# Kernel tuning notes

Measured on AMD Instinct MI355X. Metric: run time of the kernel, lower is better.

## Reference

```python
import jax, jax.numpy as jnp
import numpy as np
from jax import lax

C = 128; HEADS = 16; HD = 8; EPS = 1e-5

def _conv3x3(x, w):
    return lax.conv_general_dilated(x, w, (1, 1), 'SAME', dimension_numbers=('NCHW', 'OIHW', 'NCHW'))

def _cbr3(x, w, g, b):
    # Conv3x3 + BatchNorm(eval, running stats folded -> per-channel affine) + ReLU
    return jax.nn.relu(_conv3x3(x, w) * g[:, None, None] + b[:, None, None])

def _cbr1(x, w, g, b):
    y = jnp.einsum('bchw,oc->bohw', x, w)
    return jax.nn.relu(y * g[:, None, None] + b[:, None, None])

def _ln(t, g, b):
    mu = t.mean(-1, keepdims=True)
    va = ((t - mu) ** 2).mean(-1, keepdims=True)
    return (t - mu) / jnp.sqrt(va + EPS) * g + b

def _gconv1x1(xf, w, b, groups):
    # grouped 1x1 conv on flattened spatial dim: xf [B,Cin,N], w [Cout, Cin//groups]
    B, Cin, N = xf.shape
    Cout = w.shape[0]
    y = jnp.einsum('bgcn,goc->bgon', xf.reshape(B, groups, Cin // groups, N),
                   w.reshape(groups, Cout // groups, Cin // groups))
    return y.reshape(B, Cout, N) + b[:, None]

def _ss_softmax(a):
    # sign * sqrt(|a| + 1e-5) then softmax (GISSA's custom transform)
    a = jnp.sign(a) * jnp.sqrt(jnp.abs(a) + 1e-5)
    return jax.nn.softmax(a, axis=-1)

def _gissa(ximg, qkv_w, qkv_b, g, b, qkv2_w, qkv2_b):
    B, Cc, H, W = ximg.shape
    N = H * W
    xf = ximg.reshape(B, Cc, N)
    qkv = _gconv1x1(xf, qkv_w, qkv_b, HEADS).reshape(B, 3, HEADS, HD, N)
    q, k, v = qkv[:, 0], qkv[:, 1], qkv[:, 2]
    attn = _ss_softmax(jnp.einsum('bhdn,bhen->bhde', q, k) * HD ** -0.5)  # [B,h,hd,hd]
    x1 = jnp.einsum('bhde,bhen->bhdn', attn, v).reshape(B, Cc, N) + xf
    x1 = x1.reshape(B, HEADS, HD, N).transpose(0, 2, 1, 3).reshape(B, Cc, N)  # channel shuffle
    y = x1 * g[:, None] + b[:, None]  # BatchNorm eval affine
    xr = jax.nn.relu(y)
    qkv2 = _gconv1x1(xr, qkv2_w, qkv2_b, HD).reshape(B, 3, HD, HEADS, N)
    q2, k2, v2 = qkv2[:, 0], qkv2[:, 1], qkv2[:, 2]
    attn2 = _ss_softmax(jnp.einsum('bdhn,bdgn->bdhg', q2, k2) * HEADS ** -0.5)  # [B,hd,h,h]
    o = jnp.einsum('bdhg,bdgn->bdhn', attn2, v2).transpose(0, 2, 1, 3).reshape(B, Cc, N) + y
    return o.reshape(B, Cc, H, W)

def _swsa_calc(ximg, pi_w, pi_b, g, b, po_w, po_b):
    B, Cc, H, W = ximg.shape
    t = jnp.einsum('bcn,oc->bon', ximg.reshape(B, Cc, H * W), pi_w) + pi_b[:, None]
    t = t * g[:, None] + b[:, None]  # BN affine
    q = t[:, :Cc].transpose(0, 2, 1)  # [B,N,C]
    v = t[:, Cc:].transpose(0, 2, 1)
    atn = jax.nn.softmax(jnp.einsum('bnc,bmc->bnm', q, q) * Cc ** -0.5, axis=-1)
    y = jnp.einsum('bnm,bmc->bnc', atn, v).transpose(0, 2, 1)  # [B,C,N]
    y = (jnp.einsum('bcn,oc->bon', y, po_w) + po_b[:, None]).reshape(B, Cc, H, W)
    return y, atn

def _swsa_reuse(ximg, atn, pi_w, pi_b, g, b, po_w, po_b):
    B, Cc, H, W = ximg.shape
    t = jnp.einsum('bcn,oc->bon', ximg.reshape(B, Cc, H * W), pi_w) + pi_b[:, None]
    t = t * g[:, None] + b[:, None]
    v = t.transpose(0, 2, 1)
    y = (jnp.einsum('bnm,bmc->bnc', atn, v) * Cc ** -0.5).transpose(0, 2, 1)
    return (jnp.einsum('bcn,oc->bon', y, po_w) + po_b[:, None]).reshape(B, Cc, H, W)

def _forward(x, ssfe_w, ssfe_g, ssfe_b, cc_w, cc_g, cc_b, ln1_g, ln1_b, qkv_w, qkv_b, gbn_g, gbn_b, qkv2_w, qkv2_b, ln2_g, ln2_b, mlp_w1, mlp_b1, mlp_w2, mlp_b2, cs_w, cs_g, cs_b, lfe0_w, lfe0_g, lfe0_b, s0_pi_w, s0_pi_b, s0_bn_g, s0_bn_b, s0_po_w, s0_po_b, lfe1_w, lfe1_g, lfe1_b, s1_pi_w, s1_pi_b, s1_bn_g, s1_bn_b, s1_po_w, s1_po_b, lamuda, fc_w):
    B, Cin, H, W = x.shape
    N = H * W
    # SSFE stem (approximated as Conv3x3+BN+ReLU; source def unavailable)
    xs = _cbr3(x, ssfe_w, ssfe_g, ssfe_b)
    # channel branch: 1x1 CBR + SIT (LN -> GISSA -> residual -> LN -> MLP -> residual)
    xc = _cbr1(xs, cc_w, cc_g, cc_b)
    t = xc.reshape(B, C, N).transpose(0, 2, 1)  # [B,N,C]
    cur = _ln(t, ln1_g, ln1_b).transpose(0, 2, 1).reshape(B, C, H, W)
    t = t + _gissa(cur, qkv_w, qkv_b, gbn_g, gbn_b, qkv2_w, qkv2_b).reshape(B, C, N).transpose(0, 2, 1)
    h = _ln(t, ln2_g, ln2_b)
    h = jax.nn.gelu(h @ mlp_w1.T + mlp_b1, approximate=False) @ mlp_w2.T + mlp_b2
    t = t + h
    xc = t.transpose(0, 2, 1).reshape(B, C, H, W)
    # spatial branch: 3x3 CBR + SCA (LFE + SWSA with attention reuse)
    xp = _cbr3(xs, cs_w, cs_g, cs_b)
    xp = _cbr3(xp, lfe0_w, lfe0_g, lfe0_b) + xp
    y, atn = _swsa_calc(xp, s0_pi_w, s0_pi_b, s0_bn_g, s0_bn_b, s0_po_w, s0_po_b)
    xp = y + xp
    xp = _cbr3(xp, lfe1_w, lfe1_g, lfe1_b) + xp
    xp = _swsa_reuse(xp, atn, s1_pi_w, s1_pi_b, s1_bn_g, s1_bn_b, s1_po_w, s1_po_b) + xp
    lmd = jax.nn.sigmoid(lamuda[0])
    out = lmd * xc + (1.0 - lmd) * xp
    return out.mean(axis=(2, 3)) @ fc_w.T  # global avg pool + fc (dropout p=0 for HUST2013)

def setup_inputs():
    ks = iter(jax.random.split(jax.random.key(0), 64))
    def rn(shape, scale=0.05):
        return jax.random.normal(next(ks), shape, jnp.float32) * scale
    ones = lambda *s: jnp.ones(s, jnp.float32)
    zeros = lambda *s: jnp.zeros(s, jnp.float32)
    return dict(
        x=jax.random.normal(next(ks), (32, 144, 32, 32), jnp.float32),
        ssfe_w=rn((144, 144, 3, 3)), ssfe_g=ones(144), ssfe_b=zeros(144),
        cc_w=rn((128, 144)), cc_g=ones(128), cc_b=zeros(128),
        ln1_g=ones(128), ln1_b=zeros(128),
        qkv_w=rn((384, 8)), qkv_b=zeros(384),
        gbn_g=ones(128), gbn_b=zeros(128),
        qkv2_w=rn((384, 16)), qkv2_b=zeros(384),
        ln2_g=ones(128), ln2_b=zeros(128),
        mlp_w1=rn((512, 128)), mlp_b1=zeros(512),
        mlp_w2=rn((128, 512)), mlp_b2=zeros(128),
        cs_w=rn((128, 144, 3, 3)), cs_g=ones(128), cs_b=zeros(128),
        lfe0_w=rn((128, 128, 3, 3)), lfe0_g=ones(128), lfe0_b=zeros(128),
        s0_pi_w=rn((256, 128)), s0_pi_b=zeros(256), s0_bn_g=ones(256), s0_bn_b=zeros(256),
        s0_po_w=rn((128, 128)), s0_po_b=zeros(128),
        lfe1_w=rn((128, 128, 3, 3)), lfe1_g=ones(128), lfe1_b=zeros(128),
        s1_pi_w=rn((128, 128)), s1_pi_b=zeros(128), s1_bn_g=ones(128), s1_bn_b=zeros(128),
        s1_po_w=rn((128, 128)), s1_po_b=zeros(128),
        lamuda=jnp.full((1,), 0.5, jnp.float32),
        fc_w=rn((16, 128)),
    )

def reference(x, ssfe_w, ssfe_g, ssfe_b, cc_w, cc_g, cc_b, ln1_g, ln1_b, qkv_w, qkv_b, gbn_g, gbn_b, qkv2_w, qkv2_b, ln2_g, ln2_b, mlp_w1, mlp_b1, mlp_w2, mlp_b2, cs_w, cs_g, cs_b, lfe0_w, lfe0_g, lfe0_b, s0_pi_w, s0_pi_b, s0_bn_g, s0_bn_b, s0_po_w, s0_po_b, lfe1_w, lfe1_g, lfe1_b, s1_pi_w, s1_pi_b, s1_bn_g, s1_bn_b, s1_po_w, s1_po_b, lamuda, fc_w):
    return _forward(x, ssfe_w, ssfe_g, ssfe_b, cc_w, cc_g, cc_b, ln1_g, ln1_b, qkv_w, qkv_b, gbn_g, gbn_b, qkv2_w, qkv2_b, ln2_g, ln2_b, mlp_w1, mlp_b1, mlp_w2, mlp_b2, cs_w, cs_g, cs_b, lfe0_w, lfe0_g, lfe0_b, s0_pi_w, s0_pi_b, s0_bn_g, s0_bn_b, s0_po_w, s0_po_b, lfe1_w, lfe1_g, lfe1_b, s1_pi_w, s1_pi_b, s1_bn_g, s1_bn_b, s1_po_w, s1_po_b, lamuda, fc_w)
```

## Files before the change

### kernel.cpp

```cpp
#include <hip/hip_runtime.h>
#include <math.h>


static constexpr int NPIX = 1024;

typedef __attribute__((ext_vector_type(8))) short bf16x8;
typedef __attribute__((ext_vector_type(4))) float f32x4;
typedef __attribute__((ext_vector_type(8))) unsigned short u16x8;
typedef __attribute__((ext_vector_type(4))) unsigned short u16x4;

static __device__ __forceinline__ unsigned short f2bf(float f) {
    unsigned u = __builtin_bit_cast(unsigned, f);
    unsigned r = (u + 0x7fffu + ((u >> 16) & 1u)) >> 16;
    return (unsigned short)r;
}
static __device__ __forceinline__ float bf2f(unsigned short u) {
    unsigned v = ((unsigned)u) << 16;
    return __builtin_bit_cast(float, v);
}

__global__ __launch_bounds__(256) void prepack_convs(
    const float* __restrict__ ssfe_w, const float* __restrict__ cs_w,
    const float* __restrict__ lfe0_w, const float* __restrict__ lfe1_w,
    unsigned short* __restrict__ wssfe, unsigned short* __restrict__ wcs,
// ... 188 lines not shown
    __shared__ unsigned short X[130 * PITCH];
    const int tid = threadIdx.x;
    const int b = blockIdx.x, gr = blockIdx.y;
    const int pbase = gr << 6;
    const int gbase = pbase - 33;
    const int wid = tid >> 6, lane = tid & 63;
    const int ll = lane & 15, lq = lane >> 4;
    const int co0w = wid << 5;
    const unsigned short* xb = xT + ((size_t)b << 10) * CINP;

#pragma unroll 1
    for (int idx = tid; idx < 130 * NCHK; idx += 256) {
        const int row = idx / NCHK;
        const int chunk = idx - row * NCHK;
        const int gp = gbase + row;
        u16x8 v = {};
        if (gp >= 0 && gp < 1024)
            v = *(const u16x8*)(xb + (size_t)gp * CINP + chunk * 8);
        *(u16x8*)&X[row * PITCH + chunk * 8] = v;
    }
    __syncthreads();

    f32x4 acc[2][4];
#pragma unroll
    for (int i = 0; i < 2; ++i)
#pragma unroll
        for (int j = 0; j < 4; ++j)
#pragma unroll
            for (int r = 0; r < 4; ++r) acc[i][j][r] = 0.f;

#pragma unroll
    for (int tap = 0; tap < 9; ++tap) {
        const int soff = (tap / 3) * 32 + (tap % 3);
        const int dx = tap % 3;
#pragma unroll
        for (int kc = 0; kc < CINP / 32; ++kc) {
            bf16x8 bfv[4];
#pragma unroll
            for (int j = 0; j < 4; ++j) {
                const int p = j * 16 + ll;
                bf16x8 v = *(const bf16x8*)&X[(p + soff) * PITCH + kc * 32 + lq * 8];
                const bool zed = (dx == 0 && (j & 1) == 0 && ll == 0) ||
                                 (dx == 2 && (j & 1) == 1 && ll == 15);
                if (zed) { bf16x8 z = {}; v = z; }
                bfv[j] = v;
            }
            const unsigned short* wb =
                wrep + ((size_t)tap * Cout + co0w) * CINP + kc * 32 + lq * 8;
#pragma unroll
            for (int i = 0; i < 2; ++i) {
                bf16x8 af = *(const bf16x8*)(wb + (size_t)(i * 16 + ll) * CINP);
#pragma unroll
                for (int j = 0; j < 4; ++j)
                    acc[i][j] = __builtin_amdgcn_mfma_f32_16x16x32_bf16(
                        af, bfv[j], acc[i][j], 0, 0, 0);
            }
        }
    }

#pragma unroll
    for (int i = 0; i < 2; ++i) {
        const int cob = co0w + i * 16 + lq * 4;
        float gv[4], bv[4];
#pragma unroll
        for (int r = 0; r < 4; ++r) { gv[r] = g[cob + r]; bv[r] = bb[cob + r]; }
#pragma unroll
        for (int j = 0; j < 4; ++j) {
            const int px = pbase + j * 16 + ll;
            const size_t rowT = ((size_t)((b << 10) + px)) << 7;
            u16x4 rv = {};
            if (resT) rv = *(const u16x4*)(resT + rowT + cob);
            u16x4 tp;
#pragma unroll
            for (int r = 0; r < 4; ++r) {
                float v = fmaxf(acc[i][j][r] * gv[r] + bv[r], 0.f);
                if (resT) v += bf2f(rv[r]);
                tp[r] = f2bf(v);
            }
            *(u16x4*)(outT + rowT + cob) = tp;
        }
    }
}

template <int KP>
__global__ __launch_bounds__(256) void lin_mfma_kernel(
    const unsigned short* __restrict__ xT, const unsigned short* __restrict__ wbf,
    const float* __restrict__ bias0, const float* __restrict__ g,
    const float* __restrict__ bb, const unsigned short* __restrict__ resT,
    float* __restrict__ outF, unsigned short* __restrict__ outBF,
    unsigned short* __restrict__ outT, int do_relu)
{
    const int tid = threadIdx.x;
    const int b = blockIdx.x;
    const int n0 = blockIdx.y << 6;
    const int wid = tid >> 6, lane = tid & 63;
    const int ll = lane & 15, lq = lane >> 4;
    const unsigned short* xb = xT + (size_t)((b << 10) + n0) * KP;

    f32x4 acc[2][4];
#pragma unroll
    for (int i = 0; i < 2; ++i)
#pragma unroll
        for (int j = 0; j < 4; ++j)
#pragma unroll
            for (int r = 0; r < 4; ++r) acc[i][j][r] = 0.f;

#pragma unroll
    for (int kk = 0; kk < KP / 32; ++kk) {
        bf16x8 af[2], bfv[4];
#pragma unroll
        for (int i = 0; i < 2; ++i)
            af[i] = *(const bf16x8*)(wbf + (size_t)(wid * 32 + i * 16 + ll) * KP + kk * 32 + lq * 8);
#pragma unroll
        for (int j = 0; j < 4; ++j)
            bfv[j] = *(const bf16x8*)(xb + (size_t)(j * 16 + ll) * KP + kk * 32 + lq * 8);
#pragma unroll
        for (int i = 0; i < 2; ++i)
#pragma unroll
            for (int j = 0; j < 4; ++j)
                acc[i][j] = __builtin_amdgcn_mfma_f32_16x16x32_bf16(af[i], bfv[j], acc[i][j], 0, 0, 0);
    }

#pragma unroll
    for (int i = 0; i < 2; ++i) {
        const int cob = wid * 32 + i * 16 + lq * 4;
        float b0v[4], gv[4], bv[4];
#pragma unroll
        for (int r = 0; r < 4; ++r) {
            b0v[r] = bias0 ? bias0[cob + r] : 0.f;
            gv[r] = g ? g[cob + r] : 1.f;
            bv[r] = g ? bb[cob + r] : 0.f;
        }
#pragma unroll
        for (int j = 0; j < 4; ++j) {
            const int px = n0 + j * 16 + ll;
            const size_t rowT = ((size_t)((b << 10) + px)) << 7;
            u16x4 rv = {};
            if (resT) rv = *(const u16x4*)(resT + rowT + cob);
            u16x4 tp;
#pragma unroll
            for (int r = 0; r < 4; ++r) {
                const int co = cob + r;
                float v = acc[i][j][r] + b0v[r];
                v = v * gv[r] + bv[r];
                if (do_relu) v = fmaxf(v, 0.f);
                if (resT) v += bf2f(rv[r]);
                if (outF) outF[((size_t)((b << 7) + co) << 10) + px] = v;
                unsigned short h = f2bf(v);
                if (outBF) outBF[((size_t)((b << 7) + co) << 10) + px] = h;
                tp[r] = h;
            }
            if (outT) *(u16x4*)(outT + rowT + cob) = tp;
        }
    }
}

__global__ __launch_bounds__(256) void pi0_kernel(
    const unsigned short* __restrict__ xT, const unsigned short* __restrict__ wbf,
    const float* __restrict__ bias0, const float* __restrict__ g,
    const float* __restrict__ bb, unsigned short* __restrict__ qTout,
    unsigned short* __restrict__ vout)
{
    const int tid = threadIdx.x;
    const int b = blockIdx.x;
    const int n0 = blockIdx.y << 6;
    const int wid = tid >> 6, lane = tid & 63;
    const int ll = lane & 15, lq = lane >> 4;
    const int co0 = wid << 6;
    const unsigned short* xb = xT + (size_t)((b << 10) + n0) * 128;

    f32x4 acc[4][4];
#pragma unroll
    for (int i = 0; i < 4; ++i)
#pragma unroll
        for (int j = 0; j < 4; ++j)
#pragma unroll
            for (int r = 0; r < 4; ++r) acc[i][j][r] = 0.f;

#pragma unroll
    for (int kk = 0; kk < 4; ++kk) {
        bf16x8 af[4], bfv[4];
#pragma unroll
        for (int i = 0; i < 4; ++i)
            af[i] = *(const bf16x8*)(wbf + (size_t)(co0 + i * 16 + ll) * 128 + kk * 32 + lq * 8);
#pragma unroll
        for (int j = 0; j < 4; ++j)
            bfv[j] = *(const bf16x8*)(xb + (size_t)(j * 16 + ll) * 128 + kk * 32 + lq * 8);
#pragma unroll
        for (int i = 0; i < 4; ++i)
#pragma unroll
            for (int j = 0; j < 4; ++j)
                acc[i][j] = __builtin_amdgcn_mfma_f32_16x16x32_bf16(af[i], bfv[j], acc[i][j], 0, 0, 0);
    }

#pragma unroll
    for (int i = 0; i < 4; ++i) {
        const int cob = co0 + i * 16 + lq * 4;
        float b0v[4], gv[4], bv[4];
#pragma unroll
        for (int r = 0; r < 4; ++r) {
            b0v[r] = bias0[cob + r];
            gv[r] = g[cob + r];
            bv[r] = bb[cob + r];
        }
#pragma unroll
        for (int j = 0; j < 4; ++j) {
            const int px = n0 + j * 16 + ll;
            float vv[4];
#pragma unroll
            for (int r = 0; r < 4; ++r)
                vv[r] = (acc[i][j][r] + b0v[r]) * gv[r] + bv[r];
            if (wid < 2) {
                u16x4 tp;
#pragma unroll
                for (int r = 0; r < 4; ++r) tp[r] = f2bf(vv[r]);
                *(u16x4*)(qTout + (((size_t)((b << 10) + px)) << 7) + cob) = tp;
            } else {
#pragma unroll
                for (int r = 0; r < 4; ++r)
                    vout[((size_t)(b * 128 + cob - 128 + r) << 10) + px] = f2bf(vv[r]);
            }
        }
    }
}

__global__ __launch_bounds__(256) void ln_kernel(
    const float* __restrict__ in, const float* __restrict__ g,
    const float* __restrict__ bb, unsigned short* __restrict__ out_bf,
    unsigned short* __restrict__ outT)
{
    const int tid = threadIdx.x;
    const int b = blockIdx.x >> 2;
    const int n = ((blockIdx.x & 3) << 8) + tid;
    const float* ib = in + ((size_t)b << 17) + n;
    float s = 0.f, sq = 0.f;
#pragma unroll 8
    for (int c = 0; c < 128; ++c) {
        float v = ib[(size_t)c << 10];
        s += v;
        sq += v * v;
    }
    const float mu = s * 0.0078125f;
    const float r = rsqrtf(sq * 0.0078125f - mu * mu + 1e-5f);
    unsigned short* obf = out_bf + ((size_t)b << 17) + n;
    unsigned short* oT = outT + (((size_t)b << 10) + n) * 128;
#pragma unroll 2
    for (int c0 = 0; c0 < 128; c0 += 8) {
        u16x8 pk;
#pragma unroll
        for (int e = 0; e < 8; ++e) {
            const int c = c0 + e;
            float v = ib[(size_t)c << 10];
            float y = (v - mu) * r * g[c] + bb[c];
            unsigned short h = f2bf(y);
            obf[(size_t)c << 10] = h;
            pk[e] = h;
        }
        *(u16x8*)(oT + c0) = pk;
    }
}

__global__ __launch_bounds__(256) void gram_kernel(
    const unsigned short* __restrict__ Xbf, float* __restrict__ G)
{
    __shared__ unsigned short Xs[128 * 128];
    const int tid = threadIdx.x;
    const int b = blockIdx.x >> 2;
    const int rg = blockIdx.x & 3;
    const int wid = tid >> 6, lane = tid & 63;
    const int lq = lane >> 4, ll = lane & 15;
    const unsigned short* Xb = Xbf + ((size_t)b << 17);

    f32x4 acc[2][2];
#pragma unroll
    for (int mi = 0; mi < 2; ++mi)
#pragma unroll
        for (int ci = 0; ci < 2; ++ci)
#pragma unroll
            for (int r = 0; r < 4; ++r) acc[mi][ci][r] = 0.f;

#pragma unroll 1
    for (int nt = 0; nt < 8; ++nt) {
        const int n0 = nt << 7;
#pragma unroll
        for (int p = 0; p < 8; ++p) {
            const int ch = (p << 4) + (tid >> 4);
            const int seg = (tid & 15) << 3;
            *(u16x8*)&Xs[ch * 128 + (seg ^ ((ch & 7) << 3))] =
                *(const u16x8*)(Xb + ((size_t)ch << 10) + n0 + seg);
        }
        __syncthreads();
#pragma unroll
        for (int ks = 0; ks < 4; ++ks) {
            bf16x8 af[2], bf_[2];
#pragma unroll
            for (int mi = 0; mi < 2; ++mi) {
                const int ar = (rg << 5) + mi * 16 + ll;
                af[mi] = *(const bf16x8*)&Xs[ar * 128 + ((ks * 32 + lq * 8) ^ ((ar & 7) << 3))];
            }
#pragma unroll
            for (int ci = 0; ci < 2; ++ci) {
                const int br = (wid << 5) + ci * 16 + ll;
                bf_[ci] = *(const bf16x8*)&Xs[br * 128 + ((ks * 32 + lq * 8) ^ ((br & 7) << 3))];
            }
// ... 358 lines not shown
                for (int r = 0; r < 4; ++r) acc[i][j][r] = 0.f;
#pragma unroll
        for (int kk = 0; kk < 4; ++kk) {
            bf16x8 af[4], bfr[4];
#pragma unroll
            for (int i = 0; i < 4; ++i)
                af[i] = *(const bf16x8*)(w1bf + (size_t)(hidbase + i * 16 + lr) * 128 + kk * 32 + lk * 8);
#pragma unroll
            for (int j = 0; j < 4; ++j) {
                const int px = j * 16 + lr;
                bfr[j] = *(const bf16x8*)(xnb + px * 256 + ((kk * 64 + lk * 16) ^ ((px & 7) << 4)));
            }
#pragma unroll
            for (int i = 0; i < 4; ++i)
#pragma unroll
                for (int j = 0; j < 4; ++j)
                    acc[i][j] = __builtin_amdgcn_mfma_f32_16x16x32_bf16(af[i], bfr[j], acc[i][j], 0, 0, 0);
        }
#pragma unroll
        for (int i = 0; i < 4; ++i) {
            const int hid0 = hidbase + i * 16 + lk * 4;
            float bi[4];
#pragma unroll
            for (int r = 0; r < 4; ++r) bi[r] = b1[hid0 + r];
#pragma unroll
            for (int j = 0; j < 4; ++j) {
                const int px = j * 16 + lr;
                u16x4 pk;
#pragma unroll
                for (int r = 0; r < 4; ++r) {
                    float x = acc[i][j][r] + bi[r];
                    float u = 1.5957691f * x * (1.f + 0.044715f * x * x);
                    float gv = x / (1.f + __expf(-u));
                    pk[r] = f2bf(gv);
                }
                *(u16x4*)(hb + px * 1024 + ((hid0 * 2) ^ ((px & 7) << 4))) = pk;
            }
        }
    }
    __syncthreads();

    f32x4 acc2[2][4];
#pragma unroll
    for (int i = 0; i < 2; ++i)
#pragma unroll
        for (int j = 0; j < 4; ++j)
#pragma unroll
            for (int r = 0; r < 4; ++r) acc2[i][j][r] = 0.f;
#pragma unroll 2
    for (int ks = 0; ks < 16; ++ks) {
        bf16x8 af[2], bfr[4];
#pragma unroll
        for (int i = 0; i < 2; ++i)
            af[i] = *(const bf16x8*)(w2bf + (size_t)((wid << 5) + i * 16 + lr) * 512 + ks * 32 + lk * 8);
#pragma unroll
        for (int j = 0; j < 4; ++j) {
            const int px = j * 16 + lr;
            bfr[j] = *(const bf16x8*)(hb + px * 1024 + ((ks * 64 + lk * 16) ^ ((px & 7) << 4)));
        }
#pragma unroll
        for (int i = 0; i < 2; ++i)
#pragma unroll
            for (int j = 0; j < 4; ++j)
                acc2[i][j] = __builtin_amdgcn_mfma_f32_16x16x32_bf16(af[i], bfr[j], acc2[i][j], 0, 0, 0);
    }
#pragma unroll
    for (int i = 0; i < 2; ++i) {
        const int cb = (wid << 5) + i * 16 + lk * 4;
        float b2v[4];
#pragma unroll
        for (int r = 0; r < 4; ++r) b2v[r] = b2[cb + r];
#pragma unroll
        for (int j = 0; j < 4; ++j) {
            const int px = j * 16 + lr;
#pragma unroll
            for (int r = 0; r < 4; ++r) {
                const size_t off = ((size_t)(cb + r) << 10) + px;
                tb[off] += acc2[i][j][r] + b2v[r];
            }
        }
    }
}

__global__ __launch_bounds__(256) void swsa_po_kernel(
    const unsigned short* __restrict__ qT, const unsigned short* __restrict__ vbf,
    const unsigned short* __restrict__ wpo, const float* __restrict__ po_b,
    const unsigned short* __restrict__ resT,
    unsigned short* __restrict__ outT, float* __restrict__ outF, float fscale)
{
    __shared__ unsigned short K_lds[128 * 128];
    __shared__ unsigned short V_lds[128 * 128];
    const int tid = threadIdx.x;
    const int b = blockIdx.x & 31;
    const int n0 = (blockIdx.x >> 5) << 6;
    const int wid = tid >> 6, lane = tid & 63;
    const int lq = lane >> 4, ll = lane & 15;
    const unsigned short* qTb = qT + ((size_t)b << 17);
    const unsigned short* vb = vbf + ((size_t)b << 17);

    bf16x8 aq[4];
    {
        const int row = n0 + wid * 16 + ll;
#pragma unroll
        for (int kk = 0; kk < 4; ++kk)
            aq[kk] = *(const bf16x8*)(qTb + ((size_t)row << 7) + kk * 32 + lq * 8);
    }

    float mrun[4], lrun[4];
#pragma unroll
    for (int i = 0; i < 4; ++i) { mrun[i] = -INFINITY; lrun[i] = 0.f; }
    f32x4 yacc[8];
#pragma unroll
    for (int cj = 0; cj < 8; ++cj)
#pragma unroll
        for (int r = 0; r < 4; ++r) yacc[cj][r] = 0.f;

#pragma unroll 1
    for (int mt = 0; mt < 8; ++mt) {
        const int m0 = mt << 7;
        for (int ch = tid; ch < 2048; ch += 256) {
            const int rr = ch >> 4, e0 = (ch & 15) << 3;
            const int sw = (rr & 7) << 3;
            *(u16x8*)&K_lds[rr * 128 + (e0 ^ sw)] =
                *(const u16x8*)(qTb + ((size_t)(m0 + rr) << 7) + e0);
            *(u16x8*)&V_lds[rr * 128 + (e0 ^ sw)] =
                *(const u16x8*)(vb + ((size_t)rr << 10) + m0 + e0);
        }
        __syncthreads();

        f32x4 sacc[8];
#pragma unroll
        for (int j = 0; j < 8; ++j)
#pragma unroll
            for (int r = 0; r < 4; ++r) sacc[j][r] = 0.f;
#pragma unroll
        for (int j = 0; j < 8; ++j) {
            const int ml = j * 16 + ll;
            const int swk = (ml & 7) << 3;
#pragma unroll
            for (int kk = 0; kk < 4; ++kk) {
                bf16x8 bk = *(const bf16x8*)&K_lds[ml * 128 + ((kk * 32 + lq * 8) ^ swk)];
                sacc[j] = __builtin_amdgcn_mfma_f32_16x16x32_bf16(aq[kk], bk, sacc[j], 0, 0, 0);
            }
        }
        __syncthreads();

        float pmax[4];
#pragma unroll
        for (int i = 0; i < 4; ++i) pmax[i] = -INFINITY;
#pragma unroll
        for (int j = 0; j < 8; ++j)
#pragma unroll
            for (int r = 0; r < 4; ++r) {
                float s = sacc[j][r] * 0.08838834764831845f;
                sacc[j][r] = s;
                pmax[r] = fmaxf(pmax[r], s);
            }
        float alpha[4];
#pragma unroll
        for (int i = 0; i < 4; ++i) {
            float m = pmax[i];
            m = fmaxf(m, __shfl_xor(m, 1));
            m = fmaxf(m, __shfl_xor(m, 2));
            m = fmaxf(m, __shfl_xor(m, 4));
            m = fmaxf(m, __shfl_xor(m, 8));
            const float mn = fmaxf(mrun[i], m);
            alpha[i] = __expf(mrun[i] - mn);
            mrun[i] = mn;
        }
        float psum[4];
#pragma unroll
        for (int r = 0; r < 4; ++r) {
            const int nbw = wid * 16 + lq * 4 + r;
            const int sw4 = ((nbw >> 2) & 3) << 4;
            const float mn = mrun[r];
            float ps = 0.f;
#pragma unroll
            for (int j = 0; j < 8; ++j) {
                float p = __expf(sacc[j][r] - mn);
                ps += p;
                K_lds[nbw * 128 + ((j * 16 + ll) ^ sw4)] = f2bf(p);
            }
            psum[r] = ps;
        }
#pragma unroll
        for (int i = 0; i < 4; ++i) {
            float s = psum[i];
            s += __shfl_xor(s, 1);
            s += __shfl_xor(s, 2);
            s += __shfl_xor(s, 4);
            s += __shfl_xor(s, 8);
            lrun[i] = lrun[i] * alpha[i] + s;
        }
#pragma unroll
        for (int cj = 0; cj < 8; ++cj)
#pragma unroll
            for (int r = 0; r < 4; ++r) yacc[cj][r] *= alpha[r];

        bf16x8 ap[4];
        {
            const int nb = wid * 16 + ll;
            const int sw4 = ((nb >> 2) & 3) << 4;
#pragma unroll
            for (int mk = 0; mk < 4; ++mk)
                ap[mk] = *(const bf16x8*)&K_lds[nb * 128 + ((mk * 32 + lq * 8) ^ sw4)];
        }
#pragma unroll
        for (int cj = 0; cj < 8; ++cj) {
            const int cl = cj * 16 + ll;
            const int sw = (cl & 7) << 3;
#pragma unroll
            for (int mk = 0; mk < 4; ++mk) {
                bf16x8 bv = *(const bf16x8*)&V_lds[cl * 128 + ((mk * 32 + lq * 8) ^ sw)];
                yacc[cj] = __builtin_amdgcn_mfma_f32_16x16x32_bf16(ap[mk], bv, yacc[cj], 0, 0, 0);
            }
        }
        __syncthreads();
    }

    {
        float inv[4];
#pragma unroll
        for (int r = 0; r < 4; ++r) inv[r] = fscale / lrun[r];
        const int rw0 = wid * 16 + lq * 4;
#pragma unroll
        for (int cj = 0; cj < 8; ++cj) {
            const int c = cj * 16 + ll;
#pragma unroll
            for (int r = 0; r < 4; ++r) {
                const int row = rw0 + r;
                const int sw4 = ((row >> 2) & 3) << 4;
                K_lds[row * 128 + (c ^ sw4)] = f2bf(yacc[cj][r] * inv[r]);
            }
        }
    }
    __syncthreads();

    f32x4 acc2[2][4];
#pragma unroll
    for (int i = 0; i < 2; ++i)
#pragma unroll
        for (int j = 0; j < 4; ++j)
#pragma unroll
            for (int r = 0; r < 4; ++r) acc2[i][j][r] = 0.f;
#pragma unroll
    for (int kk = 0; kk < 4; ++kk) {
        bf16x8 af[2], bfv[4];
#pragma unroll
        for (int i = 0; i < 2; ++i)
            af[i] = *(const bf16x8*)(wpo + (size_t)(wid * 32 + i * 16 + ll) * 128 + kk * 32 + lq * 8);
#pragma unroll
        for (int j = 0; j < 4; ++j) {
            const int row = j * 16 + ll;
            const int sw4 = ((row >> 2) & 3) << 4;
            bfv[j] = *(const bf16x8*)&K_lds[row * 128 + ((kk * 32 + lq * 8) ^ sw4)];
        }
#pragma unroll
        for (int i = 0; i < 2; ++i)
#pragma unroll
            for (int j = 0; j < 4; ++j)
                acc2[i][j] = __builtin_amdgcn_mfma_f32_16x16x32_bf16(af[i], bfv[j], acc2[i][j], 0, 0, 0);
    }

#pragma unroll
    for (int i = 0; i < 2; ++i) {
        const int cob = wid * 32 + i * 16 + lq * 4;
        float pob[4];
#pragma unroll
        for (int r = 0; r < 4; ++r) pob[r] = po_b[cob + r];
#pragma unroll
        for (int j = 0; j < 4; ++j) {
            const int px = n0 + j * 16 + ll;
            const size_t rowT = ((size_t)((b << 10) + px)) << 7;
            u16x4 rv = *(const u16x4*)(resT + rowT + cob);
            float vv[4];
#pragma unroll
            for (int r = 0; r < 4; ++r)
                vv[r] = acc2[i][j][r] + pob[r] + bf2f(rv[r]);
            if (outT) {
                u16x4 tp;
#pragma unroll
                for (int r = 0; r < 4; ++r) tp[r] = f2bf(vv[r]);
                *(u16x4*)(outT + rowT + cob) = tp;
            }
            if (outF) {
#pragma unroll
                for (int r = 0; r < 4; ++r)
                    outF[((size_t)(b * 128 + cob + r) << 10) + px] = vv[r];
            }
        }
    }
}

__global__ __launch_bounds__(256) void mean_kernel(
    const float* __restrict__ xc, const float* __restrict__ xp,
    const float* __restrict__ lamuda, float* __restrict__ meanb)
{
    const int wid = threadIdx.x >> 6, lane = threadIdx.x & 63;
    const int row = (blockIdx.x << 2) + wid;
    const float lmd = 1.f / (1.f + __expf(-lamuda[0]));
// ... 14 lines not shown

__global__ __launch_bounds__(256) void fc_kernel(
    const float* __restrict__ meanb, const float* __restrict__ fc_w,
    float* __restrict__ outp)
{
    const int idx = blockIdx.x * 256 + threadIdx.x;
    if (idx >= 512) return;
    const int b = idx >> 4, o = idx & 15;
    float s = 0.f;
#pragma unroll 4
    for (int c = 0; c < 128; ++c) s += fc_w[o * 128 + c] * meanb[b * 128 + c];
    outp[b * 16 + o] = s;
}

extern "C" void kernel_launch(void* const* d_in, const int* in_sizes, int n_in,
                              void* d_out, int out_size, void* d_ws, size_t ws_size,
                              hipStream_t stream)
{
    (void)in_sizes; (void)n_in; (void)out_size; (void)ws_size;

    const float* x       = (const float*)d_in[0];
    const float* ssfe_w  = (const float*)d_in[1];
    const float* ssfe_g  = (const float*)d_in[2];
    const float* ssfe_b  = (const float*)d_in[3];
    const float* cc_w    = (const float*)d_in[4];
    const float* cc_g    = (const float*)d_in[5];
    const float* cc_b    = (const float*)d_in[6];
    const float* ln1_g   = (const float*)d_in[7];
    const float* ln1_b   = (const float*)d_in[8];
    const float* qkv_w   = (const float*)d_in[9];
    const float* qkv_b   = (const float*)d_in[10];
    const float* gbn_g   = (const float*)d_in[11];
    const float* gbn_b   = (const float*)d_in[12];
    const float* qkv2_w  = (const float*)d_in[13];
    const float* qkv2_b  = (const float*)d_in[14];
    const float* ln2_g   = (const float*)d_in[15];
    const float* ln2_b   = (const float*)d_in[16];
    const float* mlp_w1  = (const float*)d_in[17];
    const float* mlp_b1  = (const float*)d_in[18];
    const float* mlp_w2  = (const float*)d_in[19];
    const float* mlp_b2  = (const float*)d_in[20];
    const float* cs_w    = (const float*)d_in[21];
    const float* cs_g    = (const float*)d_in[22];
    const float* cs_b    = (const float*)d_in[23];
    const float* lfe0_w  = (const float*)d_in[24];
    const float* lfe0_g  = (const float*)d_in[25];
    const float* lfe0_b  = (const float*)d_in[26];
    const float* s0_pi_w = (const float*)d_in[27];
    const float* s0_pi_b = (const float*)d_in[28];
    const float* s0_bn_g = (const float*)d_in[29];
    const float* s0_bn_b = (const float*)d_in[30];
    const float* s0_po_w = (const float*)d_in[31];
    const float* s0_po_b = (const float*)d_in[32];
    const float* lfe1_w  = (const float*)d_in[33];
    const float* lfe1_g  = (const float*)d_in[34];
    const float* lfe1_b  = (const float*)d_in[35];
    const float* s1_pi_w = (const float*)d_in[36];
    const float* s1_pi_b = (const float*)d_in[37];
    const float* s1_bn_g = (const float*)d_in[38];
    const float* s1_bn_b = (const float*)d_in[39];
    const float* s1_po_w = (const float*)d_in[40];
    const float* s1_po_b = (const float*)d_in[41];
    const float* lamuda  = (const float*)d_in[42];
    const float* fc_w    = (const float*)d_in[43];
    float* out = (float*)d_out;
    float* ws = (float*)d_ws;

    float* xs = ws;
    float* t  = ws + 4718592;
    float* Qr = ws + 13107200;
    float* P2 = ws + 25690112;
    float* P3 = ws + 29884416;

    unsigned short* xT0 = (unsigned short*)Qr;

    unsigned short* curbf = (unsigned short*)Qr;
    unsigned short* curT  = (unsigned short*)(Qr + 2097152);
    unsigned short* yrbf  = (unsigned short*)(Qr + 4194304);
    unsigned short* yrT   = (unsigned short*)(Qr + 6291456);
    unsigned short* xsT   = (unsigned short*)(Qr + 8388608);
    float* ybuf = P2;

    unsigned short* xpT   = (unsigned short*)Qr;
    unsigned short* qT0   = (unsigned short*)Qr;
    unsigned short* v0    = (unsigned short*)(Qr + 2097152);
    unsigned short* v1    = (unsigned short*)(Qr + 4194304);
    unsigned short* xp3T  = (unsigned short*)(Qr + 6291456);
    unsigned short* xp2T  = (unsigned short*)(Qr + 8388608);
    unsigned short* xp4T  = (unsigned short*)(Qr + 8388608);

    unsigned short* linw  = (unsigned short*)(Qr + 11010048);
    unsigned short* wcc   = linw;
    unsigned short* wpi0  = linw + 20480;
    unsigned short* wpi1  = linw + 53248;
    unsigned short* wpo0  = linw + 69632;
    unsigned short* wpo1  = linw + 86016;
    unsigned short* w1bf  = linw + 102400;
    unsigned short* w2bf  = linw + 167936;
    float* meanb = Qr + 11200000;

    float* Gbuf  = P3 + 1048576;
    float* Sbuf  = P3 + 1572864;
    unsigned short* M1bf = (unsigned short*)(P3 + 1576960);
    float* c1buf = P3 + 1839104;
    unsigned short* M2bf = (unsigned short*)(P3 + 1843200);
    float* c2buf = P3 + 2105344;

    unsigned short* wssfe = (unsigned short*)P3;
    unsigned short* wcs   = (unsigned short*)(P3 + 131072);
    unsigned short* wlfe0 = (unsigned short*)(P3 + 262144);
    unsigned short* wlfe1 = (unsigned short*)xs;

    const dim3 blk(256);

    prepack_convs<<<dim3((686592 + 255) / 256), blk, 0, stream>>>(
        ssfe_w, cs_w, lfe0_w, lfe1_w, wssfe, wcs, wlfe0, wlfe1);
    prepack_lins<<<dim3((233472 + 255) / 256), blk, 0, stream>>>(
        cc_w, s0_pi_w, s1_pi_w, s0_po_w, s1_po_w, mlp_w1, mlp_w2, linw);

    cvt_xT_kernel<<<dim3(32, 16), blk, 0, stream>>>(x, xT0);
    conv3x3_ssfe_kernel<<<dim3(32, 16), blk, 0, stream>>>(
        xT0, wssfe, ssfe_g, ssfe_b, xsT);
    lin_mfma_kernel<160><<<dim3(32, 16), blk, 0, stream>>>(
        xsT, wcc, nullptr, cc_g, cc_b, nullptr, t, nullptr, nullptr, 1);

    ln_kernel<<<dim3(128), blk, 0, stream>>>(t, ln1_g, ln1_b, curbf, curT);
    gram_kernel<<<dim3(128), blk, 0, stream>>>(curbf, Gbuf);
    sums_kernel<<<dim3(32), blk, 0, stream>>>(curbf, Sbuf);
    mats1_kernel<<<dim3(512), dim3(64), 0, stream>>>(Gbuf, Sbuf, qkv_w, qkv_b, gbn_g, gbn_b, M1bf, c1buf);
    apply1_mfma_kernel<<<dim3(256), blk, 0, stream>>>(curT, M1bf, c1buf, ybuf, yrbf, yrT);
    gram_kernel<<<dim3(128), blk, 0, stream>>>(yrbf, Gbuf);
    sums_kernel<<<dim3(32), blk, 0, stream>>>(yrbf, Sbuf);
    mats2_kernel<<<dim3(256), blk, 0, stream>>>(Gbuf, Sbuf, qkv2_w, qkv2_b, M2bf, c2buf);
    apply2_mfma_kernel<<<dim3(256), blk, 0, stream>>>(yrT, M2bf, c2buf, ybuf, t);

    mlp_mfma_kernel<<<dim3(512), blk, 0, stream>>>(t, ln2_g, ln2_b, w1bf, mlp_b1, w2bf, mlp_b2);

    conv3x3_lds_kernel<160><<<dim3(32, 16), blk, 0, stream>>>(
        xsT, wcs, cs_g, cs_b, nullptr, xpT, 128);
    conv3x3_lds_kernel<128><<<dim3(32, 16), blk, 0, stream>>>(
        xpT, wlfe0, lfe0_g, lfe0_b, xpT, xp2T, 128);
    pi0_kernel<<<dim3(32, 16), blk, 0, stream>>>(
        xp2T, wpi0, s0_pi_b, s0_bn_g, s0_bn_b, qT0, v0);
    swsa_po_kernel<<<dim3(512), blk, 0, stream>>>(
        qT0, v0, wpo0, s0_po_b, xp2T, xp3T, nullptr, 1.0f);
    conv3x3_lds_kernel<128><<<dim3(32, 16), blk, 0, stream>>>(
        xp3T, wlfe1, lfe1_g, lfe1_b, xp3T, xp4T, 128);
    lin_mfma_kernel<128><<<dim3(32, 16), blk, 0, stream>>>(
        xp4T, wpi1, s1_pi_b, s1_bn_g, s1_bn_b, nullptr, nullptr, v1, nullptr, 0);
    swsa_po_kernel<<<dim3(512), blk, 0, stream>>>(
        qT0, v1, wpo1, s1_po_b, xp4T, nullptr, P3, 0.08838834764831845f);

    mean_kernel<<<dim3(1024), blk, 0, stream>>>(t, P3, lamuda, meanb);
    fc_kernel<<<dim3(2), blk, 0, stream>>>(meanb, fc_w, out);
}
```

Before: 432.8 us.

## Fuse conv3x3 with projection-in GEMM and reuse softmax stats in second SWSA

Adds a combined kernel that runs the 3x3 conv, stages its output tile in LDS, and immediately applies the following 1x1 projection-in GEMM. This removes the separate pi0 and lin kernels and their global round trips. The first SWSA pass now saves per-row softmax max and sum, and the second pass (same Q and K) reloads them, skipping the running-max and rescale work. The cost is higher register and LDS pressure in the fused kernel. Reuse is only correct because both passes share the same Q and K, and qT0 moves to a different buffer so it outlives later writes.

```diff
diff --git a/kernel.cpp b/kernel.cpp
--- a/kernel.cpp
+++ b/kernel.cpp
@@ -294,6 +294,165 @@
     }
 }
 
+template <int PI_COUT>
+__global__ __launch_bounds__(256) void conv3x3_pi_kernel(
+    const unsigned short* __restrict__ xT,
+    const unsigned short* __restrict__ wrep,
+    const float* __restrict__ g, const float* __restrict__ bb,
+    const unsigned short* __restrict__ resT,
+    unsigned short* __restrict__ outT,
+    const unsigned short* __restrict__ wpi, const float* __restrict__ pi_b,
+    const float* __restrict__ pig, const float* __restrict__ pibb,
+    unsigned short* __restrict__ qTout, unsigned short* __restrict__ vout)
+{
+    constexpr int CINP = 128, PITCH = 136, NCHK = 16;
+    __shared__ unsigned short X[130 * PITCH];
+    unsigned short* Y = X;
+    const int tid = threadIdx.x;
+    const int b = blockIdx.x, gr = blockIdx.y;
+    const int pbase = gr << 6;
+    const int gbase = pbase - 33;
+    const int wid = tid >> 6, lane = tid & 63;
+    const int ll = lane & 15, lq = lane >> 4;
+    const int co0w = wid << 5;
+    const unsigned short* xb = xT + ((size_t)b << 10) * CINP;
+
+#pragma unroll 1
+    for (int idx = tid; idx < 130 * NCHK; idx += 256) {
+        const int row = idx / NCHK;
+        const int chunk = idx - row * NCHK;
+        const int gp = gbase + row;
+        u16x8 v = {};
+        if (gp >= 0 && gp < 1024)
+            v = *(const u16x8*)(xb + (size_t)gp * CINP + chunk * 8);
+        *(u16x8*)&X[row * PITCH + chunk * 8] = v;
+    }
+    __syncthreads();
+
+    f32x4 acc[2][4];
+#pragma unroll
+    for (int i = 0; i < 2; ++i)
+#pragma unroll
+        for (int j = 0; j < 4; ++j)
+#pragma unroll
+            for (int r = 0; r < 4; ++r) acc[i][j][r] = 0.f;
+
+#pragma unroll
+    for (int tap = 0; tap < 9; ++tap) {
+        const int soff = (tap / 3) * 32 + (tap % 3);
+        const int dx = tap % 3;
+#pragma unroll
+        for (int kc = 0; kc < CINP / 32; ++kc) {
+            bf16x8 bfv[4];
+#pragma unroll
+            for (int j = 0; j < 4; ++j) {
+                const int p = j * 16 + ll;
+                bf16x8 v = *(const bf16x8*)&X[(p + soff) * PITCH + kc * 32 + lq * 8];
+                const bool zed = (dx == 0 && (j & 1) == 0 && ll == 0) ||
+                                 (dx == 2 && (j & 1) == 1 && ll == 15);
+                if (zed) { bf16x8 z = {}; v = z; }
+                bfv[j] = v;
+            }
+            const unsigned short* wb =
+                wrep + ((size_t)tap * 128 + co0w) * CINP + kc * 32 + lq * 8;
+#pragma unroll
+            for (int i = 0; i < 2; ++i) {
+                bf16x8 af = *(const bf16x8*)(wb + (size_t)(i * 16 + ll) * CINP);
+#pragma unroll
+                for (int j = 0; j < 4; ++j)
+                    acc[i][j] = __builtin_amdgcn_mfma_f32_16x16x32_bf16(
+                        af, bfv[j], acc[i][j], 0, 0, 0);
+            }
+        }
+    }
+    __syncthreads();
+
+#pragma unroll
+    for (int i = 0; i < 2; ++i) {
+        const int cob = co0w + i * 16 + lq * 4;
+        float gv[4], bv[4];
+#pragma unroll
+        for (int r = 0; r < 4; ++r) { gv[r] = g[cob + r]; bv[r] = bb[cob + r]; }
+#pragma unroll
+        for (int j = 0; j < 4; ++j) {
+            const int pxl = j * 16 + ll;
+            const int px = pbase + pxl;
+            const size_t rowT = ((size_t)((b << 10) + px)) << 7;
+            u16x4 rv = *(const u16x4*)(resT + rowT + cob);
+            u16x4 tp;
+#pragma unroll
+            for (int r = 0; r < 4; ++r) {
+                float v = fmaxf(acc[i][j][r] * gv[r] + bv[r], 0.f) + bf2f(rv[r]);
+                tp[r] = f2bf(v);
+            }
+            *(u16x4*)(outT + rowT + cob) = tp;
+            const int sw4 = ((pxl >> 2) & 3) << 4;
+            *(u16x4*)&Y[pxl * 128 + (cob ^ sw4)] = tp;
+        }
+    }
+    __syncthreads();
+
+    constexpr int NI = PI_COUT / 64;
+    const int co0p = wid * (PI_COUT / 4);
+    f32x4 acc2[NI][4];
+#pragma unroll
+    for (int i = 0; i < NI; ++i)
+#pragma unroll
+        for (int j = 0; j < 4; ++j)
+#pragma unroll
+            for (int r = 0; r < 4; ++r) acc2[i][j][r] = 0.f;
+
+#pragma unroll
+    for (int kk = 0; kk < 4; ++kk) {
+        bf16x8 af[NI], bfv[4];
+#pragma unroll
+        for (int i = 0; i < NI; ++i)
+            af[i] = *(const bf16x8*)(wpi + (size_t)(co0p + i * 16 + ll) * 128 + kk * 32 + lq * 8);
+#pragma unroll
+        for (int j = 0; j < 4; ++j) {
+            const int pxl = j * 16 + ll;
+            const int sw4 = ((pxl >> 2) & 3) << 4;
+            bfv[j] = *(const bf16x8*)&Y[pxl * 128 + ((kk * 32 + lq * 8) ^ sw4)];
+        }
+#pragma unroll
+        for (int i = 0; i < NI; ++i)
+#pragma unroll
+            for (int j = 0; j < 4; ++j)
+                acc2[i][j] = __builtin_amdgcn_mfma_f32_16x16x32_bf16(af[i], bfv[j], acc2[i][j], 0, 0, 0);
+    }
+
+#pragma unroll
+    for (int i = 0; i < NI; ++i) {
+        const int cob = co0p + i * 16 + lq * 4;
+        float b0v[4], gv[4], bv[4];
+#pragma unroll
+        for (int r = 0; r < 4; ++r) {
+            b0v[r] = pi_b[cob + r];
+            gv[r] = pig[cob + r];
+            bv[r] = pibb[cob + r];
+        }
+#pragma unroll
+        for (int j = 0; j < 4; ++j) {
+            const int px = pbase + j * 16 + ll;
+            float vv[4];
+#pragma unroll
+            for (int r = 0; r < 4; ++r)
+                vv[r] = (acc2[i][j][r] + b0v[r]) * gv[r] + bv[r];
+            if (PI_COUT == 256 && cob < 128) {
+                u16x4 tp;
+#pragma unroll
+                for (int r = 0; r < 4; ++r) tp[r] = f2bf(vv[r]);
+                *(u16x4*)(qTout + (((size_t)((b << 10) + px)) << 7) + cob) = tp;
+            } else {
+                const int cv = (PI_COUT == 256) ? cob - 128 : cob;
+#pragma unroll
+                for (int r = 0; r < 4; ++r)
+                    vout[((size_t)(b * 128 + cv + r) << 10) + px] = f2bf(vv[r]);
+            }
+        }
+    }
+}
+
 template <int KP>
 __global__ __launch_bounds__(256) void lin_mfma_kernel(
     const unsigned short* __restrict__ xT, const unsigned short* __restrict__ wbf,
@@ -363,75 +522,6 @@
                 tp[r] = h;
             }
             if (outT) *(u16x4*)(outT + rowT + cob) = tp;
-        }
-    }
-}
-
-__global__ __launch_bounds__(256) void pi0_kernel(
-    const unsigned short* __restrict__ xT, const unsigned short* __restrict__ wbf,
-    const float* __restrict__ bias0, const float* __restrict__ g,
-    const float* __restrict__ bb, unsigned short* __restrict__ qTout,
-    unsigned short* __restrict__ vout)
-{
-    const int tid = threadIdx.x;
-    const int b = blockIdx.x;
-    const int n0 = blockIdx.y << 6;
-    const int wid = tid >> 6, lane = tid & 63;
-    const int ll = lane & 15, lq = lane >> 4;
-    const int co0 = wid << 6;
-    const unsigned short* xb = xT + (size_t)((b << 10) + n0) * 128;
-
-    f32x4 acc[4][4];
-#pragma unroll
-    for (int i = 0; i < 4; ++i)
-#pragma unroll
-        for (int j = 0; j < 4; ++j)
-#pragma unroll
-            for (int r = 0; r < 4; ++r) acc[i][j][r] = 0.f;
-
-#pragma unroll
-    for (int kk = 0; kk < 4; ++kk) {
-        bf16x8 af[4], bfv[4];
-#pragma unroll
-        for (int i = 0; i < 4; ++i)
-            af[i] = *(const bf16x8*)(wbf + (size_t)(co0 + i * 16 + ll) * 128 + kk * 32 + lq * 8);
-#pragma unroll
-        for (int j = 0; j < 4; ++j)
-            bfv[j] = *(const bf16x8*)(xb + (size_t)(j * 16 + ll) * 128 + kk * 32 + lq * 8);
-#pragma unroll
-        for (int i = 0; i < 4; ++i)
-#pragma unroll
-            for (int j = 0; j < 4; ++j)
-                acc[i][j] = __builtin_amdgcn_mfma_f32_16x16x32_bf16(af[i], bfv[j], acc[i][j], 0, 0, 0);
-    }
-
-#pragma unroll
-    for (int i = 0; i < 4; ++i) {
-        const int cob = co0 + i * 16 + lq * 4;
-        float b0v[4], gv[4], bv[4];
-#pragma unroll
-        for (int r = 0; r < 4; ++r) {
-            b0v[r] = bias0[cob + r];
-            gv[r] = g[cob + r];
-            bv[r] = bb[cob + r];
-        }
-#pragma unroll
-        for (int j = 0; j < 4; ++j) {
-            const int px = n0 + j * 16 + ll;
-            float vv[4];
-#pragma unroll
-            for (int r = 0; r < 4; ++r)
-                vv[r] = (acc[i][j][r] + b0v[r]) * gv[r] + bv[r];
-            if (wid < 2) {
-                u16x4 tp;
-#pragma unroll
-                for (int r = 0; r < 4; ++r) tp[r] = f2bf(vv[r]);
-                *(u16x4*)(qTout + (((size_t)((b << 10) + px)) << 7) + cob) = tp;
-            } else {
-#pragma unroll
-                for (int r = 0; r < 4; ++r)
-                    vout[((size_t)(b * 128 + cob - 128 + r) << 10) + px] = f2bf(vv[r]);
-            }
         }
     }
 }
@@ -956,11 +1046,13 @@
     }
 }
 
+template <int REUSE>
 __global__ __launch_bounds__(256) void swsa_po_kernel(
     const unsigned short* __restrict__ qT, const unsigned short* __restrict__ vbf,
     const unsigned short* __restrict__ wpo, const float* __restrict__ po_b,
     const unsigned short* __restrict__ resT,
-    unsigned short* __restrict__ outT, float* __restrict__ outF, float fscale)
+    unsigned short* __restrict__ outT, float* __restrict__ outF, float fscale,
+    float* __restrict__ statsM, float* __restrict__ statsL)
 {
     __shared__ unsigned short K_lds[128 * 128];
     __shared__ unsigned short V_lds[128 * 128];
@@ -971,6 +1063,7 @@
     const int lq = lane >> 4, ll = lane & 15;
     const unsigned short* qTb = qT + ((size_t)b << 17);
     const unsigned short* vb = vbf + ((size_t)b << 17);
+    const int rowbase = n0 + wid * 16 + lq * 4;
 
     bf16x8 aq[4];
     {
@@ -981,8 +1074,16 @@
     }
 
     float mrun[4], lrun[4];
-#pragma unroll
-    for (int i = 0; i < 4; ++i) { mrun[i] = -INFINITY; lrun[i] = 0.f; }
+    if (REUSE) {
+#pragma unroll
+        for (int r = 0; r < 4; ++r) {
+            mrun[r] = statsM[(b << 10) + rowbase + r];
+            lrun[r] = statsL[(b << 10) + rowbase + r];
+        }
+    } else {
+#pragma unroll
+        for (int i = 0; i < 4; ++i) { mrun[i] = -INFINITY; lrun[i] = 0.f; }
+    }
     f32x4 yacc[8];
 #pragma unroll
     for (int cj = 0; cj < 8; ++cj)
@@ -1019,57 +1120,71 @@
         }
         __syncthreads();
 
-        float pmax[4];
-#pragma unroll
-        for (int i = 0; i < 4; ++i) pmax[i] = -INFINITY;
-#pragma unroll
-        for (int j = 0; j < 8; ++j)
+        if (REUSE) {
 #pragma unroll
             for (int r = 0; r < 4; ++r) {
-                float s = sacc[j][r] * 0.08838834764831845f;
-                sacc[j][r] = s;
-                pmax[r] = fmaxf(pmax[r], s);
-            }
-        float alpha[4];
-#pragma unroll
-        for (int i = 0; i < 4; ++i) {
-            float m = pmax[i];
-            m = fmaxf(m, __shfl_xor(m, 1));
-            m = fmaxf(m, __shfl_xor(m, 2));
-            m = fmaxf(m, __shfl_xor(m, 4));
-            m = fmaxf(m, __shfl_xor(m, 8));
-            const float mn = fmaxf(mrun[i], m);
-            alpha[i] = __expf(mrun[i] - mn);
-            mrun[i] = mn;
-        }
-        float psum[4];
-#pragma unroll
-        for (int r = 0; r < 4; ++r) {
-            const int nbw = wid * 16 + lq * 4 + r;
-            const int sw4 = ((nbw >> 2) & 3) << 4;
-            const float mn = mrun[r];
-            float ps = 0.f;
-#pragma unroll
-            for (int j = 0; j < 8; ++j) {
-                float p = __expf(sacc[j][r] - mn);
-                ps += p;
-                K_lds[nbw * 128 + ((j * 16 + ll) ^ sw4)] = f2bf(p);
-            }
-            psum[r] = ps;
-        }
-#pragma unroll
-        for (int i = 0; i < 4; ++i) {
-            float s = psum[i];
-            s += __shfl_xor(s, 1);
-            s += __shfl_xor(s, 2);
-            s += __shfl_xor(s, 4);
-            s += __shfl_xor(s, 8);
-            lrun[i] = lrun[i] * alpha[i] + s;
-        }
-#pragma unroll
-        for (int cj = 0; cj < 8; ++cj)
-#pragma unroll
-            for (int r = 0; r < 4; ++r) yacc[cj][r] *= alpha[r];
+                const int nbw = wid * 16 + lq * 4 + r;
+                const int sw4 = ((nbw >> 2) & 3) << 4;
+                const float mn = mrun[r];
+#pragma unroll
+                for (int j = 0; j < 8; ++j) {
+                    float p = __expf(sacc[j][r] * 0.08838834764831845f - mn);
+                    K_lds[nbw * 128 + ((j * 16 + ll) ^ sw4)] = f2bf(p);
+                }
+            }
+        } else {
+            float pmax[4];
+#pragma unroll
+            for (int i = 0; i < 4; ++i) pmax[i] = -INFINITY;
+#pragma unroll
+            for (int j = 0; j < 8; ++j)
+#pragma unroll
+                for (int r = 0; r < 4; ++r) {
+                    float s = sacc[j][r] * 0.08838834764831845f;
+                    sacc[j][r] = s;
+                    pmax[r] = fmaxf(pmax[r], s);
+                }
+            float alpha[4];
+#pragma unroll
+            for (int i = 0; i < 4; ++i) {
+                float m = pmax[i];
+                m = fmaxf(m, __shfl_xor(m, 1));
+                m = fmaxf(m, __shfl_xor(m, 2));
+                m = fmaxf(m, __shfl_xor(m, 4));
+                m = fmaxf(m, __shfl_xor(m, 8));
+                const float mn = fmaxf(mrun[i], m);
+                alpha[i] = __expf(mrun[i] - mn);
+                mrun[i] = mn;
+            }
+            float psum[4];
+#pragma unroll
+            for (int r = 0; r < 4; ++r) {
+                const int nbw = wid * 16 + lq * 4 + r;
+                const int sw4 = ((nbw >> 2) & 3) << 4;
+                const float mn = mrun[r];
+                float ps = 0.f;
+#pragma unroll
+                for (int j = 0; j < 8; ++j) {
+                    float p = __expf(sacc[j][r] - mn);
+                    ps += p;
+                    K_lds[nbw * 128 + ((j * 16 + ll) ^ sw4)] = f2bf(p);
+                }
+                psum[r] = ps;
+            }
+#pragma unroll
+            for (int i = 0; i < 4; ++i) {
+                float s = psum[i];
+                s += __shfl_xor(s, 1);
+                s += __shfl_xor(s, 2);
+                s += __shfl_xor(s, 4);
+                s += __shfl_xor(s, 8);
+                lrun[i] = lrun[i] * alpha[i] + s;
+            }
+#pragma unroll
+            for (int cj = 0; cj < 8; ++cj)
+#pragma unroll
+                for (int r = 0; r < 4; ++r) yacc[cj][r] *= alpha[r];
+        }
 
         bf16x8 ap[4];
         {
@@ -1090,6 +1205,16 @@
             }
         }
         __syncthreads();
+    }
+
+    if (!REUSE) {
+        if (ll == 0) {
+#pragma unroll
+            for (int r = 0; r < 4; ++r) {
+                statsM[(b << 10) + rowbase + r] = mrun[r];
+                statsL[(b << 10) + rowbase + r] = lrun[r];
+            }
+        }
     }
 
     {
@@ -1270,12 +1395,12 @@
     float* ybuf = P2;
 
     unsigned short* xpT   = (unsigned short*)Qr;
-    unsigned short* qT0   = (unsigned short*)Qr;
     unsigned short* v0    = (unsigned short*)(Qr + 2097152);
     unsigned short* v1    = (unsigned short*)(Qr + 4194304);
     unsigned short* xp3T  = (unsigned short*)(Qr + 6291456);
     unsigned short* xp2T  = (unsigned short*)(Qr + 8388608);
     unsigned short* xp4T  = (unsigned short*)(Qr + 8388608);
+    unsigned short* qT0   = (unsigned short*)P2;
 
     unsigned short* linw  = (unsigned short*)(Qr + 11010048);
     unsigned short* wcc   = linw;
@@ -1285,7 +1410,9 @@
     unsigned short* wpo1  = linw + 86016;
     unsigned short* w1bf  = linw + 102400;
     unsigned short* w2bf  = linw + 167936;
-    float* meanb = Qr + 11200000;
+    float* meanb  = Qr + 11200000;
+    float* statsM = Qr + 11204096;
+    float* statsL = Qr + 11236864;
 
     float* Gbuf  = P3 + 1048576;
     float* Sbuf  = P3 + 1572864;
@@ -1326,18 +1453,16 @@
 
     conv3x3_lds_kernel<160><<<dim3(32, 16), blk, 0, stream>>>(
         xsT, wcs, cs_g, cs_b, nullptr, xpT, 128);
-    conv3x3_lds_kernel<128><<<dim3(32, 16), blk, 0, stream>>>(
-        xpT, wlfe0, lfe0_g, lfe0_b, xpT, xp2T, 128);
-    pi0_kernel<<<dim3(32, 16), blk, 0, stream>>>(
-        xp2T, wpi0, s0_pi_b, s0_bn_g, s0_bn_b, qT0, v0);
-    swsa_po_kernel<<<dim3(512), blk, 0, stream>>>(
-        qT0, v0, wpo0, s0_po_b, xp2T, xp3T, nullptr, 1.0f);
-    conv3x3_lds_kernel<128><<<dim3(32, 16), blk, 0, stream>>>(
-        xp3T, wlfe1, lfe1_g, lfe1_b, xp3T, xp4T, 128);
-    lin_mfma_kernel<128><<<dim3(32, 16), blk, 0, stream>>>(
-        xp4T, wpi1, s1_pi_b, s1_bn_g, s1_bn_b, nullptr, nullptr, v1, nullptr, 0);
-    swsa_po_kernel<<<dim3(512), blk, 0, stream>>>(
-        qT0, v1, wpo1, s1_po_b, xp4T, nullptr, P3, 0.08838834764831845f);
+    conv3x3_pi_kernel<256><<<dim3(32, 16), blk, 0, stream>>>(
+        xpT, wlfe0, lfe0_g, lfe0_b, xpT, xp2T,
+        wpi0, s0_pi_b, s0_bn_g, s0_bn_b, qT0, v0);
+    swsa_po_kernel<0><<<dim3(512), blk, 0, stream>>>(
+        qT0, v0, wpo0, s0_po_b, xp2T, xp3T, nullptr, 1.0f, statsM, statsL);
+    conv3x3_pi_kernel<128><<<dim3(32, 16), blk, 0, stream>>>(
+        xp3T, wlfe1, lfe1_g, lfe1_b, xp3T, xp4T,
+        wpi1, s1_pi_b, s1_bn_g, s1_bn_b, nullptr, v1);
+    swsa_po_kernel<1><<<dim3(512), blk, 0, stream>>>(
+        qT0, v1, wpo1, s1_po_b, xp4T, nullptr, P3, 0.08838834764831845f, statsM, statsL);
 
     mean_kernel<<<dim3(1024), blk, 0, stream>>>(t, P3, lamuda, meanb);
     fc_kernel<<<dim3(2), blk, 0, stream>>>(meanb, fc_w, out);
```

After: 423.6 us. -2.1%, faster.
